# Kernel tuning notes

Measured on AMD Instinct MI355X. Metric: run time of the kernel, lower is better.

Reference implementation:

```python
import jax, jax.numpy as jnp
import numpy as np

B, T, D_IN, H, D_OUT, L = 256, 512, 64, 512, 1, 2


def _lstm_layer(xs, W_ih, W_hh, b):
    """xs: [T, B, D]; W_ih: [4H, D]; W_hh: [4H, H]; b: [4H] (b_ih + b_hh).
    PyTorch gate order: i, f, g, o. Returns (ys [T,B,H], h_T [B,H])."""
    Bsz = xs.shape[1]
    Hh = W_hh.shape[1]
    h0 = jnp.zeros((Bsz, Hh), xs.dtype)
    c0 = jnp.zeros((Bsz, Hh), xs.dtype)

    def step(carry, x_t):
        h, c = carry
        gates = x_t @ W_ih.T + h @ W_hh.T + b  # [B, 4H]
        i, f, g, o = jnp.split(gates, 4, axis=-1)
        i = jax.nn.sigmoid(i)
        f = jax.nn.sigmoid(f)
        g = jnp.tanh(g)
        o = jax.nn.sigmoid(o)
        c = f * c + i * g
        h = o * jnp.tanh(c)
        return (h, c), h

    (hT, _), ys = jax.lax.scan(step, (h0, c0), xs)
    return ys, hT


def setup_inputs() -> dict:
    key = jax.random.key(0)
    ks = jax.random.split(key, 12)
    s = 0.05  # small init to avoid gate saturation
    return {
        "x": jax.random.normal(ks[0], (B, T, D_IN), jnp.float32),
        "W_ih0": jax.random.normal(ks[1], (4 * H, D_IN), jnp.float32) * s,
        "W_hh0": jax.random.normal(ks[2], (4 * H, H), jnp.float32) * s,
        "b0": jax.random.normal(ks[3], (4 * H,), jnp.float32) * s,
        "W_ih1": jax.random.normal(ks[4], (4 * H, H), jnp.float32) * s,
        "W_hh1": jax.random.normal(ks[5], (4 * H, H), jnp.float32) * s,
        "b1": jax.random.normal(ks[6], (4 * H,), jnp.float32) * s,
        "fc1_w": jax.random.normal(ks[7], (H, H), jnp.float32) * s,
        "fc1_b": jax.random.normal(ks[8], (H,), jnp.float32) * s,
        "fc_w": jax.random.normal(ks[9], (D_OUT, H), jnp.float32) * s,
        "fc_b": jax.random.normal(ks[10], (D_OUT,), jnp.float32) * s,
    }


def reference(x, W_ih0, W_hh0, b0, W_ih1, W_hh1, b1, fc1_w, fc1_b, fc_w, fc_b):
    xs = jnp.swapaxes(x, 0, 1)  # [T, B, D_IN]
    ys0, _ = _lstm_layer(xs, W_ih0, W_hh0, b0)      # [T, B, H]
    _, hT = _lstm_layer(ys0, W_ih1, W_hh1, b1)      # [B, H] == out[:, -1, :]
    h = jax.nn.relu(hT @ fc1_w.T + fc1_b)
    out = jax.nn.relu(h @ fc_w.T + fc_b)
    return out
```

## Files before the change

kernel.cpp:

```cpp
#include <hip/hip_runtime.h>
#include <stdint.h>


typedef __bf16 bf16;
typedef bf16  bf16x8 __attribute__((ext_vector_type(8)));
typedef float f32x4  __attribute__((ext_vector_type(4)));
typedef unsigned int u32;
typedef unsigned long long u64;

#define NB   256
#define NT   512
#define NDIN 64
#define NH   512
#define POLL_GUARD (1 << 20)
#define SLOT_BYTES ((size_t)NB * NH * 2)

static constexpr size_t OFF_XB   = 0;
static constexpr size_t OFF_WB0  = OFF_XB  + (size_t)NB*NT*NDIN*2;
static constexpr size_t OFF_WI0  = OFF_WB0 + (size_t)2048*512*2;
static constexpr size_t OFF_WI1  = OFF_WI0 + (size_t)2048*64*2;
static constexpr size_t OFF_WHS1 = OFF_WI1 + (size_t)2048*512*2;
static constexpr size_t OFF_Y0R  = OFF_WHS1+ (size_t)16*128*512*2;
static constexpr size_t OFF_R1   = OFF_Y0R + 2*SLOT_BYTES;
static constexpr size_t OFF_HT   = OFF_R1  + 2*SLOT_BYTES;
static constexpr size_t OFF_FLG  = OFF_HT  + (size_t)NB*NH*4;
static constexpr size_t WS_NEED  = OFF_FLG + 65536;

#define MFMA16(a,b,c) __builtin_amdgcn_mfma_f32_16x16x32_bf16(a,b,c,0,0,0)

__device__ __forceinline__ float fsigm(float x) {
    return __builtin_amdgcn_rcpf(1.0f + __builtin_amdgcn_exp2f(x * -1.442695041f));
}
__device__ __forceinline__ float ftanh(float x) {
    return 1.0f - 2.0f * __builtin_amdgcn_rcpf(1.0f + __builtin_amdgcn_exp2f(x * 2.885390082f));
}
__device__ __forceinline__ u32 pack_bf16(float a, float b) {
    union { bf16 h[2]; u32 u; } un;
    un.h[0] = (bf16)a; un.h[1] = (bf16)b;
    return un.u;
}
__device__ __forceinline__ bf16x8 asf(int4 x) {
    union { int4 i; bf16x8 v; } u; u.i = x; return u.v;
}

__device__ __forceinline__ void ld4_issue(const void* p0, const void* p1,
                                          const void* p2, const void* p3,
                                          int4& a, int4& b, int4& c, int4& d) {
    asm volatile(
        "global_load_dwordx4 %0, %4, off sc0 sc1\n\t"
        "global_load_dwordx4 %1, %5, off sc0 sc1\n\t"
        "global_load_dwordx4 %2, %6, off sc0 sc1\n\t"
        "global_load_dwordx4 %3, %7, off sc0 sc1"
        : "=&v"(a), "=&v"(b), "=&v"(c), "=&v"(d)
        : "v"(p0), "v"(p1), "v"(p2), "v"(p3)
        : "memory");
}
__device__ __forceinline__ void st64_cohr(void* p, u64 v) {
    asm volatile("global_store_dwordx2 %0, %1, off sc0 sc1" :: "v"(p), "v"(v) : "memory");
}
__device__ __forceinline__ void vm_drain() {
    asm volatile("s_waitcnt vmcnt(0)" ::: "memory");
    __builtin_amdgcn_sched_barrier(0);
}
__device__ __forceinline__ void ld_fence() {
    asm volatile("" ::: "memory");
    __builtin_amdgcn_sched_barrier(0);
}
__device__ __forceinline__ void poll64(const u32* f, u32 target) {
    int guard = 0;
    while (__hip_atomic_load(f, __ATOMIC_RELAXED, __HIP_MEMORY_SCOPE_AGENT) < target)
        if (++guard > POLL_GUARD) break;
}
__device__ __forceinline__ void ast32(u32* p, u32 v) {
    __hip_atomic_store(p, v, __ATOMIC_RELAXED, __HIP_MEMORY_SCOPE_AGENT);
}

__device__ __forceinline__ int wslot(int lr) {
    return ((lr >> 5) & 3) | (((lr >> 1) & 3) << 2);
}

__global__ void xcvt_kernel(const float* __restrict__ x, char* __restrict__ ws) {
    size_t i = ((size_t)blockIdx.x * 256 + threadIdx.x) * 8;
    float4 a = *(const float4*)(x + i);
    float4 b = *(const float4*)(x + i + 4);
    u32 p0 = pack_bf16(a.x, a.y), p1 = pack_bf16(a.z, a.w);
    u32 p2 = pack_bf16(b.x, b.y), p3 = pack_bf16(b.z, b.w);
    *(int4*)(ws + OFF_XB + i * 2) = make_int4((int)p0, (int)p1, (int)p2, (int)p3);
}

__global__ void prep_kernel(const float* __restrict__ Wih0f, const float* __restrict__ Whh0f,
                            const float* __restrict__ Wih1f, const float* __restrict__ Whh1f,
                            char* __restrict__ ws) {
    int idx = blockIdx.x * 256 + threadIdx.x;
    ((bf16*)(ws + OFF_WB0))[idx] = (bf16)Whh0f[idx];
    ((bf16*)(ws + OFF_WI1))[idx] = (bf16)Wih1f[idx];
    if (idx < 2048 * 64) ((bf16*)(ws + OFF_WI0))[idx] = (bf16)Wih0f[idx];
    int slice = idx >> 16;
    int lr    = (idx >> 9) & 127;
    int k     = idx & 511;
    int grow  = (lr >> 5) * 512 + slice * 32 + (lr & 31);
    ((bf16*)(ws + OFF_WHS1))[(size_t)slice * 65536 + lr * 512 + (k ^ (wslot(lr) << 3))] =
        (bf16)Whh1f[(size_t)grow * 512 + k];
}

__global__ __attribute__((amdgpu_waves_per_eu(1, 1))) __launch_bounds__(256)
void lstm_fused(const float* __restrict__ b0, const float* __restrict__ b1,
                char* __restrict__ ws) {
    extern __shared__ char smem[];
    char* WhLds = smem;
    char* hbufY = smem + 131072;
    char* hbufH = smem + 147456;

    const int tid = threadIdx.x;
    const int v = tid >> 6, l = tid & 63;
    const int l15 = l & 15, lhi = l >> 4, g = l & 3, csel = l15 >> 2;
    const int group = blockIdx.x >> 4, htile = blockIdx.x & 15;
    const int b0r = group * 16, hs = htile * 32;

    const bf16* xb = (const bf16*)(ws + OFF_XB);
    char* y0r = ws + OFF_Y0R;
    char* r1  = ws + OFF_R1;
    float* hT = (float*)(ws + OFF_HT);
    u32* FL = (u32*)(ws + OFF_FLG);
    const u32* myLine = FL + ((size_t)group * 16 + htile) * 64;
    u32* peerF        = FL + (size_t)group * 1024 + htile * 4 + v;

    {
        const char* wsrc = ws + OFF_WHS1 + (size_t)htile * 131072;
#pragma unroll
        for (int i = 0; i < 32; ++i) {
            int off = (tid + i * 256) * 16;
            *(int4*)(WhLds + off) = *(const int4*)(wsrc + off);
        }
    }

    const int wrow0 = g * 512 + hs + 8 * v + 2 * csel;
    const int wrow1 = wrow0 + 1;

    const bf16* wb0p = (const bf16*)(ws + OFF_WB0);
    const bf16* wi0p = (const bf16*)(ws + OFF_WI0);
    const bf16* wi1p = (const bf16*)(ws + OFF_WI1);
    int4 wb0[16][2], wib1[16][2];
#pragma unroll
    for (int kk = 0; kk < 16; ++kk) {
        wb0[kk][0]  = *(const int4*)(wb0p + (size_t)wrow0 * NH + kk * 32 + lhi * 8);
        wb0[kk][1]  = *(const int4*)(wb0p + (size_t)wrow1 * NH + kk * 32 + lhi * 8);
        wib1[kk][0] = *(const int4*)(wi1p + (size_t)wrow0 * NH + kk * 32 + lhi * 8);
        wib1[kk][1] = *(const int4*)(wi1p + (size_t)wrow1 * NH + kk * 32 + lhi * 8);
    }
    int4 wib0[2][2];
#pragma unroll
    for (int kk = 0; kk < 2; ++kk) {
        wib0[kk][0] = *(const int4*)(wi0p + (size_t)wrow0 * NDIN + kk * 32 + lhi * 8);
        wib0[kk][1] = *(const int4*)(wi0p + (size_t)wrow1 * NDIN + kk * 32 + lhi * 8);
    }
    const float b00 = b0[wrow0], b01 = b0[wrow1];
    const float b10 = b1[wrow0], b11 = b1[wrow1];

    float cA0[4] = {0,0,0,0}, cA1[4] = {0,0,0,0};
    float cB0[4] = {0,0,0,0}, cB1[4] = {0,0,0,0};
    f32x4 aL00, aL01, aL10, aL11;
    const int qb = l & 60;
    const int srcl = csel * 16 + g;
    const int swz = (l15 & 7) << 4;
    const int lr0 = g * 32 + 8 * v + 2 * csel;
    const int wsw = wslot(lr0) << 4;
    const int r0 = tid >> 6;
    const int bc = (tid & 63) * 16;

    int4 G0, G1, G2, G3;
    int4 H0, H1, H2, H3;

    auto issueG = [&](int slot) {
        const char* p = y0r + (size_t)slot * SLOT_BYTES + (size_t)b0r * 1024
                      + (size_t)r0 * 1024 + bc;
        ld4_issue(p, p + 4096, p + 8192, p + 12288, G0, G1, G2, G3);
    };
    auto issueH = [&](int slot) {
        const char* p = r1 + (size_t)slot * SLOT_BYTES + (size_t)b0r * 1024
                      + (size_t)r0 * 1024 + bc;
        ld4_issue(p, p + 4096, p + 8192, p + 12288, H0, H1, H2, H3);
    };
    auto ldsWrite = [&](char* buf, int4 A, int4 B, int4 C, int4 D) {
        *(int4*)(buf + (r0     ) * 1024 + (bc ^ (( r0      & 7) << 4))) = A;
        *(int4*)(buf + (r0 +  4) * 1024 + (bc ^ (((r0 + 4) & 7) << 4))) = B;
        *(int4*)(buf + (r0 +  8) * 1024 + (bc ^ (( r0      & 7) << 4))) = C;
        *(int4*)(buf + (r0 + 12) * 1024 + (bc ^ (((r0 + 4) & 7) << 4))) = D;
    };
    auto xproj0 = [&](int t) {
        const bf16* xp = xb + ((size_t)(b0r + l15) * NT + t) * NDIN + lhi * 8;
        bf16x8 xa0 = *(const bf16x8*)xp;
        bf16x8 xa1 = *(const bf16x8*)(xp + 32);
        aL00 = f32x4{b00, b00, b00, b00};
        aL01 = f32x4{b01, b01, b01, b01};
        aL00 = MFMA16(xa0, asf(wib0[0][0]), aL00); aL00 = MFMA16(xa1, asf(wib0[1][0]), aL00);
        aL01 = MFMA16(xa0, asf(wib0[0][1]), aL01); aL01 = MFMA16(xa1, asf(wib0[1][1]), aL01);
    };
    auto combine = [&](const f32x4& a0, const f32x4& a1, float* cc0, float* cc1,
                       float& h0s, float& h1s) {
        h0s = 0.f; h1s = 0.f;
#pragma unroll
        for (int j = 0; j < 4; ++j) {
            float va = a0[j];
            float gi = __shfl(va, qb), gf = __shfl(va, qb + 1);
            float gc = __shfl(va, qb + 2), go = __shfl(va, qb + 3);
            float cn = fsigm(gf) * cc0[j] + fsigm(gi) * ftanh(gc);
            cc0[j] = cn;
            float h = fsigm(go) * ftanh(cn);
            if (j == g) h0s = h;
            float vb = a1[j];
            gi = __shfl(vb, qb); gf = __shfl(vb, qb + 1);
            gc = __shfl(vb, qb + 2); go = __shfl(vb, qb + 3);
            cn = fsigm(gf) * cc1[j] + fsigm(gi) * ftanh(gc);
            cc1[j] = cn;
            h = fsigm(go) * ftanh(cn);
            if (j == g) h1s = h;
        }
    };
    auto publish = [&](float h0s, float h1s, char* tileBase) {
        u32 pk = pack_bf16(h0s, h1s);
        u32 w0 = __shfl(pk, srcl),     w1 = __shfl(pk, srcl + 4);
        u32 w2 = __shfl(pk, srcl + 8), w3 = __shfl(pk, srcl + 12);
        if (l < 16) {
            char* rp = tileBase + (size_t)l * 1024 + hs * 2 + v * 16;
            union { u32 w[2]; u64 q; } qa, qb2;
            qa.w[0] = w0; qa.w[1] = w1; qb2.w[0] = w2; qb2.w[1] = w3;
            st64_cohr(rp, qa.q); st64_cohr(rp + 8, qb2.q);
        }
    };
    auto setF = [&](u32 val) {
        if (l < 16) ast32(peerF + (size_t)l * 64, val);
    };

    __syncthreads();

    xproj0(0);
    {
        float h0s, h1s;
        combine(aL00, aL01, cA0, cA1, h0s, h1s);
        publish(h0s, h1s, y0r + (size_t)b0r * 1024);
        vm_drain();
        setF(1u);
        xproj0(1);
    }

    for (int e = 1; e <= NT; ++e) {
        const bool doL0 = (e < NT);
        const bool doH1 = (e >= 2);

        poll64(myLine + l, (u32)e);
        ld_fence();
        issueG((e - 1) & 1);
        if (doH1) issueH(e & 1);
        vm_drain();

        __syncthreads();
        ldsWrite(hbufY, G0, G1, G2, G3);
        if (doH1) ldsWrite(hbufH, H0, H1, H2, H3);
        __syncthreads();

        aL10 = f32x4{b10, b10, b10, b10};
        aL11 = f32x4{b11, b11, b11, b11};
#pragma unroll
        for (int kk = 0; kk < 16; ++kk) {
            bf16x8 ha = *(const bf16x8*)(hbufY + l15 * 1024 + ((kk * 64 + lhi * 16) ^ swz));
            if (doL0) {
                aL00 = MFMA16(ha, asf(wb0[kk][0]), aL00);
                aL01 = MFMA16(ha, asf(wb0[kk][1]), aL01);
            }
            aL10 = MFMA16(ha, asf(wib1[kk][0]), aL10);
            aL11 = MFMA16(ha, asf(wib1[kk][1]), aL11);
        }

        if (doL0) {
            float h0s, h1s;
            combine(aL00, aL01, cA0, cA1, h0s, h1s);
            publish(h0s, h1s, y0r + (size_t)(e & 1) * SLOT_BYTES + (size_t)b0r * 1024);
        }

        if (doH1) {
#pragma unroll
            for (int kk = 0; kk < 16; ++kk) {
                int kb = kk * 64 + lhi * 16;
                bf16x8 a  = *(const bf16x8*)(hbufH + l15 * 1024 + (kb ^ swz));
                bf16x8 w0 = *(const bf16x8*)(WhLds + (size_t) lr0      * 1024 + (kb ^ wsw));
                bf16x8 w1 = *(const bf16x8*)(WhLds + (size_t)(lr0 + 1) * 1024 + (kb ^ wsw));
                aL10 = MFMA16(a, w0, aL10);
                aL11 = MFMA16(a, w1, aL11);
            }
        }

        {
            float h0s, h1s;
            combine(aL10, aL11, cB0, cB1, h0s, h1s);
            if (e < NT) {
                publish(h0s, h1s, r1 + (size_t)((e - 1) & 1) * SLOT_BYTES + (size_t)b0r * 1024);
            } else {
                float* hp = hT + (size_t)(b0r + lhi * 4 + g) * NH + hs + 8 * v + 2 * csel;
                hp[0] = h0s; hp[1] = h1s;
            }
        }
        if (e < NT) {
            vm_drain();
            setF((u32)(e + 1));
            xproj0(e + 1);
        }
    }
}

__global__ __launch_bounds__(256) void fc_kernel(const float* __restrict__ fc1_w,
                                                 const float* __restrict__ fc1_b,
                                                 const float* __restrict__ fc_w,
                                                 const float* __restrict__ fc_b,
                                                 const char* __restrict__ ws,
                                                 float* __restrict__ out) {
    __shared__ float hLds[512];
    __shared__ float red[256];
    const int b = blockIdx.x, tid = threadIdx.x;
    const float* hT = (const float*)(ws + OFF_HT) + (size_t)b * NH;
    hLds[tid]       = hT[tid];
    hLds[tid + 256] = hT[tid + 256];
    __syncthreads();
    float p = 0.f;
#pragma unroll
    for (int rep = 0; rep < 2; ++rep) {
        int hh = tid + rep * 256;
        const float* wr = fc1_w + (size_t)hh * 512;
        float s = fc1_b[hh];
        for (int k = 0; k < 512; k += 4) {
            float4 w4 = *(const float4*)(wr + k);
            s += hLds[k] * w4.x + hLds[k + 1] * w4.y + hLds[k + 2] * w4.z + hLds[k + 3] * w4.w;
        }
        s = fmaxf(s, 0.f);
        p += s * fc_w[hh];
    }
    red[tid] = p;
    __syncthreads();
    for (int off = 128; off > 0; off >>= 1) {
        if (tid < off) red[tid] += red[tid + off];
        __syncthreads();
    }
    if (tid == 0) out[b] = fmaxf(red[0] + fc_b[0], 0.f);
}

extern "C" void kernel_launch(void* const* d_in, const int* in_sizes, int n_in,
                              void* d_out, int out_size, void* d_ws, size_t ws_size,
                              hipStream_t stream) {
    const float* x    = (const float*)d_in[0];
    const float* Wih0 = (const float*)d_in[1];
    const float* Whh0 = (const float*)d_in[2];
    const float* b0   = (const float*)d_in[3];
    const float* Wih1 = (const float*)d_in[4];
    const float* Whh1 = (const float*)d_in[5];
    const float* b1   = (const float*)d_in[6];
    const float* fc1w = (const float*)d_in[7];
    const float* fc1b = (const float*)d_in[8];
    const float* fcw  = (const float*)d_in[9];
    const float* fcb  = (const float*)d_in[10];
    char* ws = (char*)d_ws;
    float* out = (float*)d_out;

    if (ws_size < WS_NEED) {
        (void)hipMemsetAsync(d_out, 0, (size_t)out_size * 4, stream);
        return;
    }

    (void)hipMemsetAsync(ws + OFF_FLG, 0, 65536, stream);

    hipLaunchKernelGGL(xcvt_kernel, dim3(4096), dim3(256), 0, stream, x, ws);
    hipLaunchKernelGGL(prep_kernel, dim3(4096), dim3(256), 0, stream,
                       Wih0, Whh0, Wih1, Whh1, ws);
    hipLaunchKernelGGL(lstm_fused, dim3(256), dim3(256), 163840, stream, b0, b1, ws);
    hipLaunchKernelGGL(fc_kernel, dim3(256), dim3(256), 0, stream,
                       fc1w, fc1b, fcw, fcb, ws, out);
}
```

Before: 3.030 ms.

## Split layer-0 and layer-1 readiness flags to decouple the wavefront pipeline

Replaces the single per-step readiness flag with two flag sets, one for layer-0 output (Y) and one for layer-1 hidden state (H). Each block now publishes its layer-0 result and sets the Y flag before running the layer-1 recurrent MFMAs. It waits on the H flag only after the layer-0 MFMAs are done, and prefetches the next step's Y tile while layer-1 is still computing. The goal is to take layer-1 work off the critical path of the layer-0 recurrence and overlap flag polling with compute, at the cost of more polls, drains and barriers per step and a larger flag area.

```diff
diff --git a/kernel.cpp b/kernel.cpp
--- a/kernel.cpp
+++ b/kernel.cpp
@@ -24,7 +24,7 @@
 static constexpr size_t OFF_R1   = OFF_Y0R + 2*SLOT_BYTES;
 static constexpr size_t OFF_HT   = OFF_R1  + 2*SLOT_BYTES;
 static constexpr size_t OFF_FLG  = OFF_HT  + (size_t)NB*NH*4;
-static constexpr size_t WS_NEED  = OFF_FLG + 65536;
+static constexpr size_t WS_NEED  = OFF_FLG + 131072;
 
 #define MFMA16(a,b,c) __builtin_amdgcn_mfma_f32_16x16x32_bf16(a,b,c,0,0,0)
 
@@ -122,8 +122,10 @@
     char* r1  = ws + OFF_R1;
     float* hT = (float*)(ws + OFF_HT);
     u32* FL = (u32*)(ws + OFF_FLG);
-    const u32* myLine = FL + ((size_t)group * 16 + htile) * 64;
-    u32* peerF        = FL + (size_t)group * 1024 + htile * 4 + v;
+    const u32* myLineY = FL + ((size_t)group * 16 + htile) * 64;
+    const u32* myLineH = myLineY + 16384;
+    u32* peerFY       = FL + (size_t)group * 1024 + htile * 4 + v;
+    u32* peerFH       = peerFY + 16384;
 
     {
         const char* wsrc = ws + OFF_WHS1 + (size_t)htile * 131072;
@@ -228,8 +230,8 @@
             st64_cohr(rp, qa.q); st64_cohr(rp + 8, qb2.q);
         }
     };
-    auto setF = [&](u32 val) {
-        if (l < 16) ast32(peerF + (size_t)l * 64, val);
+    auto setFlag = [&](u32* base, u32 val) {
+        if (l < 16) ast32(base + (size_t)l * 64, val);
     };
 
     __syncthreads();
@@ -240,7 +242,11 @@
         combine(aL00, aL01, cA0, cA1, h0s, h1s);
         publish(h0s, h1s, y0r + (size_t)b0r * 1024);
         vm_drain();
-        setF(1u);
+        setFlag(peerFY, 1u);
+        poll64(myLineY + l, 1u);
+        ld_fence();
+        issueG(0);
+        vm_drain();
         xproj0(1);
     }
 
@@ -248,15 +254,8 @@
         const bool doL0 = (e < NT);
         const bool doH1 = (e >= 2);
 
-        poll64(myLine + l, (u32)e);
-        ld_fence();
-        issueG((e - 1) & 1);
-        if (doH1) issueH(e & 1);
-        vm_drain();
-
         __syncthreads();
         ldsWrite(hbufY, G0, G1, G2, G3);
-        if (doH1) ldsWrite(hbufH, H0, H1, H2, H3);
         __syncthreads();
 
         aL10 = f32x4{b10, b10, b10, b10};
@@ -272,13 +271,23 @@
             aL11 = MFMA16(ha, asf(wib1[kk][1]), aL11);
         }
 
+        if (doH1) {
+            poll64(myLineH + l, (u32)(e - 1));
+            ld_fence();
+            issueH(e & 1);
+        }
+
         if (doL0) {
             float h0s, h1s;
             combine(aL00, aL01, cA0, cA1, h0s, h1s);
             publish(h0s, h1s, y0r + (size_t)(e & 1) * SLOT_BYTES + (size_t)b0r * 1024);
         }
+        vm_drain();
+        if (doL0) setFlag(peerFY, (u32)(e + 1));
 
         if (doH1) {
+            ldsWrite(hbufH, H0, H1, H2, H3);
+            __syncthreads();
 #pragma unroll
             for (int kk = 0; kk < 16; ++kk) {
                 int kb = kk * 64 + lhi * 16;
@@ -290,20 +299,24 @@
             }
         }
 
+        if (e < NT) {
+            poll64(myLineY + l, (u32)(e + 1));
+            ld_fence();
+            issueG(e & 1);
+        }
+
         {
             float h0s, h1s;
             combine(aL10, aL11, cB0, cB1, h0s, h1s);
             if (e < NT) {
                 publish(h0s, h1s, r1 + (size_t)((e - 1) & 1) * SLOT_BYTES + (size_t)b0r * 1024);
+                if (e + 1 < NT) xproj0(e + 1);
+                vm_drain();
+                setFlag(peerFH, (u32)e);
             } else {
                 float* hp = hT + (size_t)(b0r + lhi * 4 + g) * NH + hs + 8 * v + 2 * csel;
                 hp[0] = h0s; hp[1] = h1s;
             }
-        }
-        if (e < NT) {
-            vm_drain();
-            setF((u32)(e + 1));
-            xproj0(e + 1);
         }
     }
 }
@@ -365,7 +378,7 @@
         return;
     }
 
-    (void)hipMemsetAsync(ws + OFF_FLG, 0, 65536, stream);
+    (void)hipMemsetAsync(ws + OFF_FLG, 0, 131072, stream);
 
     hipLaunchKernelGGL(xcvt_kernel, dim3(4096), dim3(256), 0, stream, x, ws);
     hipLaunchKernelGGL(prep_kernel, dim3(4096), dim3(256), 0, stream,
```

After: 3.286 ms. 1.08x slower.
